# Optimization experiments

Hardware: AMD Instinct MI355X
Metric: run time of the kernel (lower is better)

Reference implementation:

```python
import jax, jax.numpy as jnp
import numpy as np

B, S, C, T, WU = 32, 8, 16, 64, 16   # batch, scatterers, candidates, time, warm-up
LSTM, FC = 128, 256                  # lstm_units, fc_units
CONCAT = WU * LSTM + (T - WU) * FC   # 14336


def setup_inputs() -> dict:
    key = jax.random.key(0)
    ks = jax.random.split(key, 16)
    w = lambda k, shape, s=0.05: (jax.random.normal(k, shape, jnp.float32) * s)
    return {
        "inputs": jax.random.normal(ks[0], (B, S, C, T, 2), jnp.float32),
        "Wi": w(ks[1], (2, 4 * LSTM)),
        "Wh": w(ks[2], (LSTM, 4 * LSTM)),
        "b_lstm": jnp.zeros((4 * LSTM,), jnp.float32),
        "Wp": w(ks[3], (LSTM, 2)),
        "bp": jnp.zeros((2,), jnp.float32),
        "W1": w(ks[4], (2, FC)),
        "b1": jnp.zeros((FC,), jnp.float32),
        "W2": w(ks[5], (FC, FC)),
        "b2": jnp.zeros((FC,), jnp.float32),
        "Wc": w(ks[6], (CONCAT, FC), 0.01),
        "bc": jnp.zeros((FC,), jnp.float32),
        "Wprob": w(ks[7], (FC, 2)),
        "bprob": jnp.zeros((2,), jnp.float32),
        "Wasso": w(ks[8], (FC, 1)),
        "basso": jnp.zeros((1,), jnp.float32),
        "warm_up_length": WU,
    }


def reference(inputs, Wi, Wh, b_lstm, Wp, bp, W1, b1, W2, b2,
              Wc, bc, Wprob, bprob, Wasso, basso, warm_up_length):
    Bb, Ss, Cc, Tt, _ = inputs.shape
    N = Bb * Ss * Cc
    Wl = int(warm_up_length)
    Tr = Tt - Wl
    U = Wh.shape[0]
    Fc = W2.shape[1]
    x = inputs.reshape(N, Tt, 2)

    def cell(carry, xt):  # Keras LSTMCell step
        h, c = carry
        z = xt @ Wi + h @ Wh + b_lstm            # [N, 4U]
        i, f, g, o = jnp.split(z, 4, axis=-1)
        c = jax.nn.sigmoid(f) * c + jax.nn.sigmoid(i) * jnp.tanh(g)
        h = jax.nn.sigmoid(o) * jnp.tanh(c)
        return (h, c), h

    h0 = jnp.zeros((N, U), inputs.dtype)
    c0 = jnp.zeros((N, U), inputs.dtype)
    # warm-up: teacher-forced steps over the first Wl frames
    (h, c), hs = jax.lax.scan(cell, (h0, c0), jnp.swapaxes(x[:, :Wl], 0, 1))
    pred = jnp.tanh(h @ Wp + bp)                  # dense_lstm_pred on last warm-up output

    def ar(carry, _):
        p, h, c = carry
        (h, c), hn = cell((h, c), p)
        p2 = jnp.tanh(hn @ Wp + bp)
        return (p2, h, c), p2

    _, preds = jax.lax.scan(ar, (pred, h, c), None, length=Tr)
    preds = jnp.swapaxes(preds, 0, 1)             # [N, Tr, 2]

    # association heads (dropout = identity at inference)
    t1 = jnp.tanh(preds @ W1 + b1)                # [N, Tr, FC]
    t2 = jnp.tanh(t1 @ W2 + b2)                   # [N, Tr, FC]
    flat_lstm = jnp.swapaxes(hs, 0, 1).reshape(N, Wl * U)
    concat = jnp.concatenate([flat_lstm, t2.reshape(N, Tr * Fc)], axis=-1)
    ev = jnp.tanh(concat @ Wc + bc)               # [N, FC]
    prob = jax.nn.softmax(ev @ Wprob + bprob, axis=-1)
    cost = ev @ Wasso + basso                     # [N, 1]

    out = jnp.zeros((4, Bb, Ss, Cc, Tr, 2), inputs.dtype)
    out = out.at[0].set(preds.reshape(Bb, Ss, Cc, Tr, 2))
    out = out.at[1, :, :, :, 0, 0].set(cost.reshape(Bb, Ss, Cc))
    out = out.at[2, :, :, :, 0].set(prob.reshape(Bb, Ss, Cc, 2))
    out = out.at[3].set(inputs[:, :, :, Wl:, :])
    return out
```

## Files before the change

kernel.cpp:

```cpp
#include <hip/hip_runtime.h>
#include <stdint.h>

typedef float  f32x4  __attribute__((ext_vector_type(4)));
typedef short  short8 __attribute__((ext_vector_type(8)));

#define DEV __device__ __forceinline__

#define L2E  1.4426950408889634f
#define L2E2 2.8853900817779268f

DEV float ex2(float x){ float r; asm("v_exp_f32 %0, %1" : "=v"(r) : "v"(x)); return r; }

DEV unsigned short f2bf(float x){
  union { float f; unsigned u; } v; v.f = x;
  unsigned r = v.u + 0x7fffu + ((v.u >> 16) & 1u);
  return (unsigned short)(r >> 16);
}
DEV float bf2f(unsigned short u){
  union { unsigned u; float f; } v; v.u = ((unsigned)u) << 16;
  return v.f;
}
DEV float tanhx_(float x){ return 1.f - 2.f*__builtin_amdgcn_rcpf(1.f + ex2(x*L2E2)); }
DEV float sig_ps(float z){ return __builtin_amdgcn_rcpf(1.f + ex2(z)); }
DEV float tanh_ps(float z){ return 1.f - 2.f*__builtin_amdgcn_rcpf(1.f + ex2(z)); }

template<bool SWZ, bool GSCALE>
__global__ void __launch_bounds__(256) transpose_bf16_k(const float* __restrict__ src,
    unsigned short* __restrict__ dst, int R, int C)
{
  __shared__ float tile[32][33];
  const int tx = threadIdx.x & 31, ty = threadIdx.x >> 5;
  const int c0 = blockIdx.x * 32, r0 = blockIdx.y * 32;
  #pragma unroll
  for (int m = 0; m < 4; ++m){
    int r = ty + m*8;
    tile[r][tx] = src[(size_t)(r0 + r) * C + (c0 + tx)];
  }
  __syncthreads();
  #pragma unroll
  for (int m = 0; m < 4; ++m){
    int cc = c0 + ty + m*8;
    int k  = r0 + tx;
    int k2 = SWZ ? (k ^ ((cc & 7) << 3)) : k;
    float v = tile[tx][ty + m*8];
    if (GSCALE) v *= ((cc >> 7) == 2) ? L2E2 : -L2E;
    dst[(size_t)cc * R + k2] = f2bf(v);
  }
}

__global__ void __launch_bounds__(256) copy_out3_k(const float* __restrict__ in,
                                                   float* __restrict__ out3)
{
  int i = blockIdx.x * 256 + threadIdx.x;
  int n = i / 24, q = i - n*24;
  f32x4 v = *(const f32x4*)(in + (size_t)n*128 + 32 + q*4);
  *(f32x4*)(out3 + (size_t)n*96 + q*4) = v;
}

__global__ void __launch_bounds__(512, 2) lstm_k(
    const float* __restrict__ inputs, const float* __restrict__ Wi,
    const unsigned short* __restrict__ WhT, const float* __restrict__ bl,
    const float* __restrict__ Wp, const float* __restrict__ bp,
    unsigned short* __restrict__ concat, float* __restrict__ out0)
{
  __shared__ __align__(16) unsigned char hbuf[2*16*16*16];
  __shared__ __align__(16) unsigned char hwu[16*16*256];
  __shared__ float predb[48][16][2];
  __shared__ float xwu[16][33];
  const int tid = threadIdx.x, lane = tid & 63, w = tid >> 6;
  const int n0 = blockIdx.x * 16;
  const int col = lane & 15;
  const int u = w*16 + col;
  const int rbase = (lane >> 4) * 4;

  { int s = tid >> 5, e = tid & 31;
    xwu[s][e] = inputs[(size_t)(n0 + s)*128 + e]; }

  short8 bfrag[4][4];
  #pragma unroll
  for (int g = 0; g < 4; ++g){
    const unsigned short* p = WhT + (size_t)(g*128 + u) * 128;
    #pragma unroll
    for (int kt = 0; kt < 4; ++kt)
      bfrag[g][kt] = *(const short8*)(p + kt*32 + (lane >> 4)*8);
  }
  short8 wpf[4];
  #pragma unroll
  for (int kt = 0; kt < 4; ++kt){
    short8 v;
    #pragma unroll
    for (int j = 0; j < 8; ++j){
      int k = kt*32 + (lane >> 4)*8 + j;
      v[j] = (short)f2bf(Wp[k*2 + (col & 1)]);
    }
    wpf[kt] = v;
  }
  float wi0[4], wi1[4], bb[4];
  #pragma unroll
  for (int g = 0; g < 4; ++g){
    int c = g*128 + u;
    float sc = (g == 2) ? L2E2 : -L2E;
    wi0[g] = Wi[c] * sc; wi1[g] = Wi[512 + c] * sc; bb[g] = bl[c] * sc;
  }
  const float bpv = bp[col & 1];
  float cst[4] = {0.f, 0.f, 0.f, 0.f};
  __syncthreads();

  #pragma unroll 1
  for (int t = 0; t < 64; ++t){
    const unsigned char* rd = hbuf + ((t + 1) & 1) * 4096;
    unsigned char*       wr = hbuf + (t & 1) * 4096;
    short8 afr[4];
    if (t > 0){
      #pragma unroll
      for (int kt = 0; kt < 4; ++kt)
        afr[kt] = *(const short8*)(rd + (kt*4 + (lane >> 4))*256 + col*16);
    }
    float x0[4], x1[4];
    if (t < 16){
      #pragma unroll
      for (int i = 0; i < 4; ++i){
        x0[i] = xwu[rbase + i][t*2]; x1[i] = xwu[rbase + i][t*2 + 1];
      }
    } else {
      f32x4 pa = {0.f,0.f,0.f,0.f}, pb = {0.f,0.f,0.f,0.f};
      pa = __builtin_amdgcn_mfma_f32_16x16x32_bf16(afr[0], wpf[0], pa, 0, 0, 0);
      pb = __builtin_amdgcn_mfma_f32_16x16x32_bf16(afr[1], wpf[1], pb, 0, 0, 0);
      pa = __builtin_amdgcn_mfma_f32_16x16x32_bf16(afr[2], wpf[2], pa, 0, 0, 0);
      pb = __builtin_amdgcn_mfma_f32_16x16x32_bf16(afr[3], wpf[3], pb, 0, 0, 0);
      float val[4];
      #pragma unroll
      for (int i = 0; i < 4; ++i) val[i] = tanhx_(pa[i] + pb[i] + bpv);
      #pragma unroll
      for (int i = 0; i < 4; ++i){
        float ov_ = __shfl_xor(val[i], 1);
        x0[i] = (col & 1) ? ov_ : val[i];
        x1[i] = (col & 1) ? val[i] : ov_;
      }
      if (w == 0 && col < 2 && t >= 17){
        #pragma unroll
        for (int i = 0; i < 4; ++i) predb[t - 17][rbase + i][col] = val[i];
      }
    }
    f32x4 accA[4], accB[4];
    #pragma unroll
    for (int g = 0; g < 4; ++g){
      accA[g] = (f32x4){bb[g], bb[g], bb[g], bb[g]};
      accB[g] = (f32x4){0.f, 0.f, 0.f, 0.f};
    }
    if (t > 0){
      #pragma unroll
      for (int g = 0; g < 4; ++g){
        accA[g] = __builtin_amdgcn_mfma_f32_16x16x32_bf16(afr[0], bfrag[g][0], accA[g], 0, 0, 0);
        accB[g] = __builtin_amdgcn_mfma_f32_16x16x32_bf16(afr[1], bfrag[g][1], accB[g], 0, 0, 0);
      }
      #pragma unroll
      for (int g = 0; g < 4; ++g){
        accA[g] = __builtin_amdgcn_mfma_f32_16x16x32_bf16(afr[2], bfrag[g][2], accA[g], 0, 0, 0);
        accB[g] = __builtin_amdgcn_mfma_f32_16x16x32_bf16(afr[3], bfrag[g][3], accB[g], 0, 0, 0);
      }
    }
    #pragma unroll
    for (int i = 0; i < 4; ++i){
      float z0 = accA[0][i] + accB[0][i] + x0[i]*wi0[0] + x1[i]*wi1[0];
      float z1 = accA[1][i] + accB[1][i] + x0[i]*wi0[1] + x1[i]*wi1[1];
      float z2 = accA[2][i] + accB[2][i] + x0[i]*wi0[2] + x1[i]*wi1[2];
      float z3 = accA[3][i] + accB[3][i] + x0[i]*wi0[3] + x1[i]*wi1[3];
      float iv = sig_ps(z0), fv = sig_ps(z1), gv = tanh_ps(z2), ov = sig_ps(z3);
      float c = fv*cst[i] + iv*gv;
      cst[i] = c;
      float hf = ov * tanhx_(c);
      unsigned short hb = f2bf(hf);
      int r = rbase + i;
      *(unsigned short*)(wr + (u >> 3)*256 + r*16 + (u & 7)*2) = hb;
      if (t < 16)
        *(unsigned short*)(hwu + t*4096 + r*256 + u*2) = hb;
    }
    __syncthreads();
  }
  {
    const unsigned char* rd = hbuf + 4096;
    short8 afr[4];
    #pragma unroll
    for (int kt = 0; kt < 4; ++kt)
      afr[kt] = *(const short8*)(rd + (kt*4 + (lane >> 4))*256 + col*16);
    f32x4 pa = {0.f,0.f,0.f,0.f}, pb = {0.f,0.f,0.f,0.f};
    pa = __builtin_amdgcn_mfma_f32_16x16x32_bf16(afr[0], wpf[0], pa, 0, 0, 0);
    pb = __builtin_amdgcn_mfma_f32_16x16x32_bf16(afr[1], wpf[1], pb, 0, 0, 0);
    pa = __builtin_amdgcn_mfma_f32_16x16x32_bf16(afr[2], wpf[2], pa, 0, 0, 0);
    pb = __builtin_amdgcn_mfma_f32_16x16x32_bf16(afr[3], wpf[3], pb, 0, 0, 0);
    if (w == 0 && col < 2){
      #pragma unroll
      for (int i = 0; i < 4; ++i) predb[47][rbase + i][col] = tanhx_(pa[i] + pb[i] + bpv);
    }
  }
  __syncthreads();
  for (int idx = tid; idx < 4096; idx += 512){
    int t = idx >> 8, s = (idx >> 4) & 15, j = idx & 15;
    short8 v = *(const short8*)(hwu + t*4096 + s*256 + j*16);
    *(short8*)((unsigned char*)concat + (size_t)(n0 + s)*28672
        + ((unsigned)(t*256 + j*16) ^ ((s & 7) << 4))) = v;
  }
  for (int idx = tid; idx < 1536; idx += 512){
    int s = idx / 96, r = idx - s*96;
    out0[(size_t)(n0 + s)*96 + r] = predb[r >> 1][s][r & 1];
  }
}

__global__ void __launch_bounds__(256) t1t2_k(
    const float* __restrict__ preds, const float* __restrict__ W1,
    const float* __restrict__ b1, const unsigned short* __restrict__ W2T,
    const float* __restrict__ b2, unsigned short* __restrict__ concat)
{
  __shared__ __align__(16) unsigned char t1buf[16*512];
  const int tid = threadIdx.x, lane = tid & 63, w = tid >> 6;

  short8 bfrag[4][8];
  {
    const int krow = (lane >> 4) * 8;
    #pragma unroll
    for (int nt = 0; nt < 4; ++nt){
      const unsigned short* p = W2T + (size_t)(w*64 + nt*16 + (lane & 15)) * 256;
      #pragma unroll
      for (int kt = 0; kt < 8; ++kt){
        bfrag[nt][kt] = *(const short8*)(p + kt*32 + krow);
      }
    }
  }
  float b2c[4];
  #pragma unroll
  for (int nt = 0; nt < 4; ++nt) b2c[nt] = b2[w*64 + nt*16 + (lane & 15)];
  float w1a[16], w1b[16], b1c[16];
  {
    const int k0 = (tid & 15) * 16;
    #pragma unroll
    for (int j = 0; j < 16; ++j){
      w1a[j] = W1[k0 + j]; w1b[j] = W1[256 + k0 + j]; b1c[j] = b1[k0 + j];
    }
  }
  const int lr = tid >> 4, k0 = (tid & 15) * 16;

  #pragma unroll 1
  for (int rt = 0; rt < 8; ++rt){
    const int r0 = blockIdx.x * 128 + rt * 16;
    {
      const float p0 = preds[(size_t)(r0 + lr)*2 + 0];
      const float p1 = preds[(size_t)(r0 + lr)*2 + 1];
      const int sw = (lr & 7) << 4;
      #pragma unroll
      for (int h = 0; h < 2; ++h){
        short8 t1v;
        #pragma unroll
        for (int j = 0; j < 8; ++j){
          int jj = h*8 + j;
          t1v[j] = (short)f2bf(tanhx_(p0*w1a[jj] + p1*w1b[jj] + b1c[jj]));
        }
        *(short8*)(t1buf + ((lr*512 + (k0 + h*8)*2) ^ sw)) = t1v;
      }
    }
    __syncthreads();
    f32x4 acc[4];
    #pragma unroll
    for (int nt = 0; nt < 4; ++nt) acc[nt] = (f32x4){0.f,0.f,0.f,0.f};
    {
      const int row = lane & 15;
      const int sw = (row & 7) << 4;
      #pragma unroll
      for (int kt = 0; kt < 8; ++kt){
        short8 a = *(const short8*)(t1buf + ((row*512 + (kt*32 + (lane>>4)*8)*2) ^ sw));
        #pragma unroll
        for (int nt = 0; nt < 4; ++nt){
          acc[nt] = __builtin_amdgcn_mfma_f32_16x16x32_bf16(a, bfrag[nt][kt], acc[nt], 0, 0, 0);
        }
      }
    }
    #pragma unroll
    for (int nt = 0; nt < 4; ++nt){
      const int col = w*64 + nt*16 + (lane & 15);
      #pragma unroll
      for (int i = 0; i < 4; ++i){
        int m = r0 + (lane >> 4)*4 + i;
        int n = m / 48, tt = m - n*48;
        unsigned short val = f2bf(tanhx_(acc[nt][i] + b2c[nt]));
        *(unsigned short*)((unsigned char*)concat + (size_t)n*28672
            + ((unsigned)((2048 + tt*256 + col)*2) ^ ((n & 7) << 4))) = val;
      }
    }
    __syncthreads();
  }
}

__global__ void __launch_bounds__(512, 2) ev_k(
    const unsigned short* __restrict__ concat, const unsigned short* __restrict__ WcT,
    float* __restrict__ partials)
{
  __shared__ __align__(16) unsigned char Abuf[128*128];
  __shared__ __align__(16) unsigned char Bbuf[256*128];
  const int tid = threadIdx.x, lane = tid & 63, w = tid >> 6;
  const int wm = w >> 2, wn = w & 3;
  const int n0 = blockIdx.x * 128;
  const int kbase = blockIdx.y * 1792;

  f32x4 acc[4][4];
  #pragma unroll
  for (int mt = 0; mt < 4; ++mt)
    #pragma unroll
    for (int nt = 0; nt < 4; ++nt) acc[mt][nt] = (f32x4){0.f,0.f,0.f,0.f};

  const int aoff = tid * 32;
  const int arow = aoff >> 7;
  const unsigned char* asrc = (const unsigned char*)concat + (size_t)(n0 + arow)*28672 + (aoff & 127);
  const int bcol = tid >> 1, bhalf = (tid & 1) * 64;
  const unsigned char* bsrc = (const unsigned char*)WcT + (size_t)bcol*28672 + bhalf;

  #pragma unroll 1
  for (int ch = 0; ch < 28; ++ch){
    const int kk2 = (kbase + ch*64) * 2;
    short8 ar0 = *(const short8*)(asrc + kk2);
    short8 ar1 = *(const short8*)(asrc + kk2 + 16);
    short8 br[4];
    #pragma unroll
    for (int kb = 0; kb < 4; ++kb) br[kb] = *(const short8*)(bsrc + kk2 + kb*16);
    __syncthreads();
    *(short8*)(Abuf + aoff)      = ar0;
    *(short8*)(Abuf + aoff + 16) = ar1;
    #pragma unroll
    for (int kb = 0; kb < 4; ++kb) *(short8*)(Bbuf + bcol*128 + bhalf + kb*16) = br[kb];
    __syncthreads();
    #pragma unroll
    for (int kt = 0; kt < 2; ++kt){
      const int kby = kt*64 + (lane >> 4)*16;
      short8 afr[4], bfr[4];
      #pragma unroll
      for (int mt = 0; mt < 4; ++mt){
        int row = wm*64 + mt*16 + (lane & 15);
        afr[mt] = *(const short8*)(Abuf + ((row*128 + kby) ^ ((row & 7) << 4)));
      }
      #pragma unroll
      for (int nt = 0; nt < 4; ++nt){
        int col = wn*64 + nt*16 + (lane & 15);
        bfr[nt] = *(const short8*)(Bbuf + ((col*128 + kby) ^ ((col & 7) << 4)));
      }
      #pragma unroll
      for (int mt = 0; mt < 4; ++mt)
        #pragma unroll
        for (int nt = 0; nt < 4; ++nt)
          acc[mt][nt] = __builtin_amdgcn_mfma_f32_16x16x32_bf16(afr[mt], bfr[nt], acc[mt][nt], 0, 0, 0);
    }
  }
  float* dst = partials + (size_t)blockIdx.y * (4096*256);
  #pragma unroll
  for (int mt = 0; mt < 4; ++mt){
    #pragma unroll
    for (int nt = 0; nt < 4; ++nt){
      #pragma unroll
      for (int i = 0; i < 4; ++i){
        int n = n0 + wm*64 + mt*16 + (lane >> 4)*4 + i;
        int col = wn*64 + nt*16 + (lane & 15);
        dst[(size_t)n*256 + col] = acc[mt][nt][i];
      }
    }
  }
}

__global__ void __launch_bounds__(256) heads_k(
    const float* __restrict__ partials, const float* __restrict__ bc,
    const float* __restrict__ Wprob, const float* __restrict__ bprob,
    const float* __restrict__ Wasso, const float* __restrict__ basso,
    float* __restrict__ out1, float* __restrict__ out2)
{
  __shared__ float evs[16][257];
  const int tid = threadIdx.x;
  const int nl = tid >> 4, part = tid & 15;
  const int n = blockIdx.x * 16 + nl;
  #pragma unroll
  for (int q = 0; q < 4; ++q){
    const int c = part*16 + q*4;
    f32x4 s = {0.f,0.f,0.f,0.f};
    #pragma unroll
    for (int p = 0; p < 8; ++p){
      s += *(const f32x4*)(partials + (size_t)p*1048576 + (size_t)n*256 + c);
    }
    #pragma unroll
    for (int j = 0; j < 4; ++j) evs[nl][c + j] = tanhx_(s[j] + bc[c + j]);
  }
  __syncthreads();
  float s0 = 0.f, s1 = 0.f, s2 = 0.f;
  #pragma unroll
  for (int j = 0; j < 16; ++j){
    int c = part*16 + j;
    float e = evs[nl][c];
    s0 += e * Wprob[c*2];
    s1 += e * Wprob[c*2 + 1];
    s2 += e * Wasso[c];
  }
  s0 += __shfl_xor(s0, 1); s1 += __shfl_xor(s1, 1); s2 += __shfl_xor(s2, 1);
  s0 += __shfl_xor(s0, 2); s1 += __shfl_xor(s1, 2); s2 += __shfl_xor(s2, 2);
  s0 += __shfl_xor(s0, 4); s1 += __shfl_xor(s1, 4); s2 += __shfl_xor(s2, 4);
  s0 += __shfl_xor(s0, 8); s1 += __shfl_xor(s1, 8); s2 += __shfl_xor(s2, 8);
  if (part == 0){
    float a0 = s0 + bprob[0], a1 = s1 + bprob[1];
    float m = fmaxf(a0, a1);
    float e0 = ex2((a0 - m)*L2E), e1 = ex2((a1 - m)*L2E);
    float inv = __builtin_amdgcn_rcpf(e0 + e1);
    out2[(size_t)n*96 + 0] = e0 * inv;
    out2[(size_t)n*96 + 1] = e1 * inv;
    out1[(size_t)n*96 + 0] = s2 + basso[0];
  }
}

extern "C" void kernel_launch(void* const* d_in, const int* in_sizes, int n_in,
                              void* d_out, int out_size, void* d_ws, size_t ws_size,
                              hipStream_t stream)
{
  (void)in_sizes; (void)n_in; (void)ws_size;
  const float* inputs = (const float*)d_in[0];
  const float* Wi     = (const float*)d_in[1];
  const float* Wh     = (const float*)d_in[2];
  const float* bl     = (const float*)d_in[3];
  const float* Wp     = (const float*)d_in[4];
  const float* bp     = (const float*)d_in[5];
  const float* W1     = (const float*)d_in[6];
  const float* b1     = (const float*)d_in[7];
  const float* W2     = (const float*)d_in[8];
  const float* b2     = (const float*)d_in[9];
  const float* Wc     = (const float*)d_in[10];
  const float* bc     = (const float*)d_in[11];
  const float* Wprob  = (const float*)d_in[12];
  const float* bprob  = (const float*)d_in[13];
  const float* Wasso  = (const float*)d_in[14];
  const float* basso  = (const float*)d_in[15];
  float* out = (float*)d_out;

  char* ws = (char*)d_ws;
  unsigned short* concat = (unsigned short*)ws;
  unsigned short* WhT    = (unsigned short*)(ws + 117440512);
  unsigned short* W2T    = (unsigned short*)(ws + 117571584);
  unsigned short* WcT    = (unsigned short*)(ws + 117702656);
  float*          parts  = (float*)(ws + 125042688);

  hipMemsetAsync(d_out, 0, (size_t)out_size * sizeof(float), stream);
  dim3 blk(256);
  transpose_bf16_k<false, true ><<<dim3(16, 4),  blk, 0, stream>>>(Wh, WhT, 128, 512);
  transpose_bf16_k<false, false><<<dim3(8, 8),   blk, 0, stream>>>(W2, W2T, 256, 256);
  transpose_bf16_k<true,  false><<<dim3(8, 448), blk, 0, stream>>>(Wc, WcT, 14336, 256);
  copy_out3_k<<<384, blk, 0, stream>>>(inputs, out + 3*393216);
  lstm_k<<<256, dim3(512), 0, stream>>>(inputs, Wi, WhT, bl, Wp, bp, concat, out);
  t1t2_k<<<1536, blk, 0, stream>>>(out, W1, b1, W2T, b2, concat);
  ev_k<<<dim3(32, 8), dim3(512), 0, stream>>>(concat, WcT, parts);
  heads_k<<<256, blk, 0, stream>>>(parts, bc, Wprob, bprob, Wasso, basso,
                                   out + 393216, out + 2*393216);
}
```

Before: 234.3 us.

## Prefetch next Wc chunk into registers and simplify LSTM MFMA accumulation

In the concat GEMM, the global loads for the next K-chunk are issued right after the shared-memory store barrier, so they overlap with the MFMA work on the current chunk (register double-buffering). In the LSTM recurrence, the split A/B accumulators are merged into a single chain seeded with the bias, and the prediction head's MFMA chain is seeded with bp. This drops several adds but lengthens the dependent MFMA chain. Hidden-state bf16 conversion now uses the packed v_cvt_pk_bf16_f32 instruction instead of manual rounding.

```diff
diff --git a/kernel.cpp b/kernel.cpp
--- a/kernel.cpp
+++ b/kernel.cpp
@@ -10,6 +10,9 @@
 #define L2E2 2.8853900817779268f
 
 DEV float ex2(float x){ float r; asm("v_exp_f32 %0, %1" : "=v"(r) : "v"(x)); return r; }
+DEV unsigned cvtpk_bf16(float lo, float hi){
+  unsigned r; asm("v_cvt_pk_bf16_f32 %0, %1, %2" : "=v"(r) : "v"(lo), "v"(hi)); return r;
+}
 
 DEV unsigned short f2bf(float x){
   union { float f; unsigned u; } v; v.f = x;
@@ -95,14 +98,18 @@
     }
     wpf[kt] = v;
   }
-  float wi0[4], wi1[4], bb[4];
+  float wi0[4], wi1[4];
+  f32x4 bbv[4];
   #pragma unroll
   for (int g = 0; g < 4; ++g){
     int c = g*128 + u;
     float sc = (g == 2) ? L2E2 : -L2E;
-    wi0[g] = Wi[c] * sc; wi1[g] = Wi[512 + c] * sc; bb[g] = bl[c] * sc;
+    wi0[g] = Wi[c] * sc; wi1[g] = Wi[512 + c] * sc;
+    float b = bl[c] * sc;
+    bbv[g] = (f32x4){b, b, b, b};
   }
   const float bpv = bp[col & 1];
+  const f32x4 bpvv = (f32x4){bpv, bpv, bpv, bpv};
   float cst[4] = {0.f, 0.f, 0.f, 0.f};
   __syncthreads();
 
@@ -123,14 +130,13 @@
         x0[i] = xwu[rbase + i][t*2]; x1[i] = xwu[rbase + i][t*2 + 1];
       }
     } else {
-      f32x4 pa = {0.f,0.f,0.f,0.f}, pb = {0.f,0.f,0.f,0.f};
-      pa = __builtin_amdgcn_mfma_f32_16x16x32_bf16(afr[0], wpf[0], pa, 0, 0, 0);
-      pb = __builtin_amdgcn_mfma_f32_16x16x32_bf16(afr[1], wpf[1], pb, 0, 0, 0);
-      pa = __builtin_amdgcn_mfma_f32_16x16x32_bf16(afr[2], wpf[2], pa, 0, 0, 0);
-      pb = __builtin_amdgcn_mfma_f32_16x16x32_bf16(afr[3], wpf[3], pb, 0, 0, 0);
+      f32x4 pacc = __builtin_amdgcn_mfma_f32_16x16x32_bf16(afr[0], wpf[0], bpvv, 0, 0, 0);
+      pacc = __builtin_amdgcn_mfma_f32_16x16x32_bf16(afr[1], wpf[1], pacc, 0, 0, 0);
+      pacc = __builtin_amdgcn_mfma_f32_16x16x32_bf16(afr[2], wpf[2], pacc, 0, 0, 0);
+      pacc = __builtin_amdgcn_mfma_f32_16x16x32_bf16(afr[3], wpf[3], pacc, 0, 0, 0);
       float val[4];
       #pragma unroll
-      for (int i = 0; i < 4; ++i) val[i] = tanhx_(pa[i] + pb[i] + bpv);
+      for (int i = 0; i < 4; ++i) val[i] = tanhx_(pacc[i]);
       #pragma unroll
       for (int i = 0; i < 4; ++i){
         float ov_ = __shfl_xor(val[i], 1);
@@ -142,39 +148,44 @@
         for (int i = 0; i < 4; ++i) predb[t - 17][rbase + i][col] = val[i];
       }
     }
-    f32x4 accA[4], accB[4];
-    #pragma unroll
-    for (int g = 0; g < 4; ++g){
-      accA[g] = (f32x4){bb[g], bb[g], bb[g], bb[g]};
-      accB[g] = (f32x4){0.f, 0.f, 0.f, 0.f};
-    }
+    f32x4 acc[4];
     if (t > 0){
       #pragma unroll
-      for (int g = 0; g < 4; ++g){
-        accA[g] = __builtin_amdgcn_mfma_f32_16x16x32_bf16(afr[0], bfrag[g][0], accA[g], 0, 0, 0);
-        accB[g] = __builtin_amdgcn_mfma_f32_16x16x32_bf16(afr[1], bfrag[g][1], accB[g], 0, 0, 0);
-      }
-      #pragma unroll
-      for (int g = 0; g < 4; ++g){
-        accA[g] = __builtin_amdgcn_mfma_f32_16x16x32_bf16(afr[2], bfrag[g][2], accA[g], 0, 0, 0);
-        accB[g] = __builtin_amdgcn_mfma_f32_16x16x32_bf16(afr[3], bfrag[g][3], accB[g], 0, 0, 0);
-      }
-    }
+      for (int g = 0; g < 4; ++g)
+        acc[g] = __builtin_amdgcn_mfma_f32_16x16x32_bf16(afr[0], bfrag[g][0], bbv[g], 0, 0, 0);
+      #pragma unroll
+      for (int kt = 1; kt < 4; ++kt){
+        #pragma unroll
+        for (int g = 0; g < 4; ++g)
+          acc[g] = __builtin_amdgcn_mfma_f32_16x16x32_bf16(afr[kt], bfrag[g][kt], acc[g], 0, 0, 0);
+      }
+    } else {
+      #pragma unroll
+      for (int g = 0; g < 4; ++g) acc[g] = bbv[g];
+    }
+    float hf[4];
     #pragma unroll
     for (int i = 0; i < 4; ++i){
-      float z0 = accA[0][i] + accB[0][i] + x0[i]*wi0[0] + x1[i]*wi1[0];
-      float z1 = accA[1][i] + accB[1][i] + x0[i]*wi0[1] + x1[i]*wi1[1];
-      float z2 = accA[2][i] + accB[2][i] + x0[i]*wi0[2] + x1[i]*wi1[2];
-      float z3 = accA[3][i] + accB[3][i] + x0[i]*wi0[3] + x1[i]*wi1[3];
+      float z0 = acc[0][i] + x0[i]*wi0[0] + x1[i]*wi1[0];
+      float z1 = acc[1][i] + x0[i]*wi0[1] + x1[i]*wi1[1];
+      float z2 = acc[2][i] + x0[i]*wi0[2] + x1[i]*wi1[2];
+      float z3 = acc[3][i] + x0[i]*wi0[3] + x1[i]*wi1[3];
       float iv = sig_ps(z0), fv = sig_ps(z1), gv = tanh_ps(z2), ov = sig_ps(z3);
       float c = fv*cst[i] + iv*gv;
       cst[i] = c;
-      float hf = ov * tanhx_(c);
-      unsigned short hb = f2bf(hf);
+      hf[i] = ov * tanhx_(c);
+    }
+    unsigned p01 = cvtpk_bf16(hf[0], hf[1]);
+    unsigned p23 = cvtpk_bf16(hf[2], hf[3]);
+    unsigned short hb[4] = {
+      (unsigned short)(p01 & 0xffffu), (unsigned short)(p01 >> 16),
+      (unsigned short)(p23 & 0xffffu), (unsigned short)(p23 >> 16) };
+    #pragma unroll
+    for (int i = 0; i < 4; ++i){
       int r = rbase + i;
-      *(unsigned short*)(wr + (u >> 3)*256 + r*16 + (u & 7)*2) = hb;
+      *(unsigned short*)(wr + (u >> 3)*256 + r*16 + (u & 7)*2) = hb[i];
       if (t < 16)
-        *(unsigned short*)(hwu + t*4096 + r*256 + u*2) = hb;
+        *(unsigned short*)(hwu + t*4096 + r*256 + u*2) = hb[i];
     }
     __syncthreads();
   }
@@ -184,14 +195,13 @@
     #pragma unroll
     for (int kt = 0; kt < 4; ++kt)
       afr[kt] = *(const short8*)(rd + (kt*4 + (lane >> 4))*256 + col*16);
-    f32x4 pa = {0.f,0.f,0.f,0.f}, pb = {0.f,0.f,0.f,0.f};
-    pa = __builtin_amdgcn_mfma_f32_16x16x32_bf16(afr[0], wpf[0], pa, 0, 0, 0);
-    pb = __builtin_amdgcn_mfma_f32_16x16x32_bf16(afr[1], wpf[1], pb, 0, 0, 0);
-    pa = __builtin_amdgcn_mfma_f32_16x16x32_bf16(afr[2], wpf[2], pa, 0, 0, 0);
-    pb = __builtin_amdgcn_mfma_f32_16x16x32_bf16(afr[3], wpf[3], pb, 0, 0, 0);
+    f32x4 pacc = __builtin_amdgcn_mfma_f32_16x16x32_bf16(afr[0], wpf[0], bpvv, 0, 0, 0);
+    pacc = __builtin_amdgcn_mfma_f32_16x16x32_bf16(afr[1], wpf[1], pacc, 0, 0, 0);
+    pacc = __builtin_amdgcn_mfma_f32_16x16x32_bf16(afr[2], wpf[2], pacc, 0, 0, 0);
+    pacc = __builtin_amdgcn_mfma_f32_16x16x32_bf16(afr[3], wpf[3], pacc, 0, 0, 0);
     if (w == 0 && col < 2){
       #pragma unroll
-      for (int i = 0; i < 4; ++i) predb[47][rbase + i][col] = tanhx_(pa[i] + pb[i] + bpv);
+      for (int i = 0; i < 4; ++i) predb[47][rbase + i][col] = tanhx_(pacc[i]);
     }
   }
   __syncthreads();
@@ -313,20 +323,27 @@
   const int bcol = tid >> 1, bhalf = (tid & 1) * 64;
   const unsigned char* bsrc = (const unsigned char*)WcT + (size_t)bcol*28672 + bhalf;
 
+  short8 ar0 = *(const short8*)(asrc + kbase*2);
+  short8 ar1 = *(const short8*)(asrc + kbase*2 + 16);
+  short8 br[4];
+  #pragma unroll
+  for (int kb = 0; kb < 4; ++kb) br[kb] = *(const short8*)(bsrc + kbase*2 + kb*16);
+
   #pragma unroll 1
   for (int ch = 0; ch < 28; ++ch){
-    const int kk2 = (kbase + ch*64) * 2;
-    short8 ar0 = *(const short8*)(asrc + kk2);
-    short8 ar1 = *(const short8*)(asrc + kk2 + 16);
-    short8 br[4];
-    #pragma unroll
-    for (int kb = 0; kb < 4; ++kb) br[kb] = *(const short8*)(bsrc + kk2 + kb*16);
     __syncthreads();
     *(short8*)(Abuf + aoff)      = ar0;
     *(short8*)(Abuf + aoff + 16) = ar1;
     #pragma unroll
     for (int kb = 0; kb < 4; ++kb) *(short8*)(Bbuf + bcol*128 + bhalf + kb*16) = br[kb];
     __syncthreads();
+    if (ch < 27){
+      const int kk2 = (kbase + (ch + 1)*64) * 2;
+      ar0 = *(const short8*)(asrc + kk2);
+      ar1 = *(const short8*)(asrc + kk2 + 16);
+      #pragma unroll
+      for (int kb = 0; kb < 4; ++kb) br[kb] = *(const short8*)(bsrc + kk2 + kb*16);
+    }
     #pragma unroll
     for (int kt = 0; kt < 2; ++kt){
       const int kby = kt*64 + (lane >> 4)*16;
```

Result: no change. 230.5 us (-1.6%).
